# Kernel optimization log

Hardware: AMD Instinct MI355X
Metric: run time of the kernel (lower is better)

## Reference

```python
import jax, jax.numpy as jnp
import numpy as np

R0 = 1.0
DIM_A, DIM_V, DIM_D = 32, 32, 32
N_NODES = 20000
N_EDGES = 640000


def radial_encode_8(r, r0):
    # 8 Gaussian radial basis functions on the edge length |r_ij|
    d = jnp.linalg.norm(r, axis=-1)                      # [E]
    centers = jnp.linspace(0.0, r0, 8)                   # [8]
    width = r0 / 8.0
    return jnp.exp(-(((d[..., None] - centers) / width) ** 2))  # [E,8]


def tens_sigmoid_vec(v):
    # norm-saturating nonlinearity for rank-1 tensors (direction-preserving)
    n2 = jnp.sum(v * v, axis=-1, keepdims=True)
    return v * jax.lax.rsqrt(1.0 + n2)


def setup_inputs() -> dict:
    key = jax.random.key(0)
    ks = jax.random.split(key, 12)

    def lin(k, fan_in, fan_out):
        return jax.random.normal(k, (fan_in, fan_out), jnp.float32) / np.float32(np.sqrt(fan_in))

    return dict(
        r_ij=jax.random.normal(ks[0], (N_EDGES, 3), jnp.float32),
        w_rad=lin(ks[1], 8, DIM_A), b_rad=jnp.zeros((DIM_A,), jnp.float32),
        w_direct=lin(ks[2], DIM_A, DIM_A),
        w1=lin(ks[3], DIM_A, 2 * DIM_A), b1=jnp.zeros((2 * DIM_A,), jnp.float32),
        w2=lin(ks[4], 2 * DIM_A, 2 * DIM_A), b2=jnp.zeros((2 * DIM_A,), jnp.float32),
        w3=lin(ks[5], 2 * DIM_A, DIM_A), b3=jnp.zeros((DIM_A,), jnp.float32),
        w_v=lin(ks[6], DIM_A, DIM_V),
        w_d=lin(ks[7], DIM_A, DIM_D),
        edges_src=jax.random.randint(ks[8], (N_EDGES,), 0, N_NODES),
        n_nodes=N_NODES,
    )


def reference(r_ij, w_rad, b_rad, w_direct, w1, b1, w2, b2, w3, b3, w_v, w_d,
              edges_src, n_nodes):
    lrelu = lambda x: jnp.where(x > 0, x, 0.1 * x)
    # radial MLP: Linear(8, a) -> MLP (lin_direct + 3-layer leakyrelu net)
    h = radial_encode_8(r_ij, R0) @ w_rad + b_rad                      # [E,a]
    rad = h @ w_direct + (lrelu(lrelu(h @ w1 + b1) @ w2 + b2) @ w3 + b3)  # [E,a]
    rs = tens_sigmoid_vec(r_ij * (7.0 / R0))                            # [E,3]

    seg = lambda x: jax.ops.segment_sum(x, edges_src, num_segments=n_nodes)
    A_a = seg(rad)                                                      # [N,a]
    A_v = seg(rad[:, :, None] * rs[:, None, :])                         # [N,a,3]
    # phi_d_ij = rad ⊗ rs ⊗ rs per edge  -> [E,a,3,3], then scatter-sum
    A_d = seg(rad[:, :, None, None] * rs[:, None, None, :] * rs[:, None, :, None])  # [N,a,3,3]

    out_v = jnp.einsum('nac,av->nvc', A_v, w_v)                         # TensLinear rank 1
    out_d = jnp.einsum('naij,ad->ndij', A_d, w_d)                       # TensLinear rank 2
    return A_a, out_v, out_d
```

## Files before the change

kernel.cpp:

```cpp
#include <hip/hip_runtime.h>
#include <hip/hip_bf16.h>
#include <hip/hip_fp16.h>
#include <math.h>


#define TSIZE 8192
#define DMAX  2.0f
#define NPB   4
#define EPB   4
#define HB    128
#define TILE  10240

#define O_WRAD 0
#define O_BRAD 256
#define O_WDIR 288
#define O_W1   1312
#define O_B1   3360
#define O_W2   3424
#define O_B2   7520
#define O_W3   7584
#define O_B3   9632
#define O_WV   9664
#define O_WD   10688
#define W_TOT  11712

__device__ __forceinline__ float lrelu(float x) { return x > 0.0f ? x : 0.1f * x; }

__device__ __forceinline__ float ldf(const void* p, int i, bool f32) {
    return f32 ? ((const float*)p)[i]
               : __uint_as_float(((unsigned int)((const unsigned short*)p)[i]) << 16);
}
__device__ __forceinline__ void stf(void* p, size_t i, float v, bool f32) {
    if (f32) ((float*)p)[i] = v;
    else     ((__hip_bfloat16*)p)[i] = __float2bfloat16(v);
}

__device__ __forceinline__ bool detect_f32(const void* r) {
    const unsigned short* p = (const unsigned short*)r;
    int bad = 0;
#pragma unroll 8
    for (int i = 0; i < 128; i++) {
        float v = __uint_as_float(((unsigned int)p[i]) << 16);
        bad |= (!isfinite(v) || fabsf(v) > 1e5f) ? 1 : 0;
    }
    return bad != 0;
}

__global__ void k_prep(const void* __restrict__ r_ij,
                       const void* w_rad, const void* b_rad, const void* w_direct,
                       const void* w1, const void* b1, const void* w2, const void* b2,
                       const void* w3, const void* b3, const void* w_v, const void* w_d,
                       float* __restrict__ wcat, int* __restrict__ flag,
                       int* __restrict__ counts, int N) {
    const int b = blockIdx.x;
    if (b == 0) {
        if (threadIdx.x == 0) flag[0] = detect_f32(r_ij) ? 1 : 0;
    } else if (b <= 11) {
        const bool f32 = detect_f32(r_ij);
        const void* src; int cnt; int off;
        switch (b) {
            case 1:  src = w_rad;    cnt = 256;  off = O_WRAD; break;
            case 2:  src = b_rad;    cnt = 32;   off = O_BRAD; break;
            case 3:  src = w_direct; cnt = 1024; off = O_WDIR; break;
            case 4:  src = w1;       cnt = 2048; off = O_W1;   break;
            case 5:  src = b1;       cnt = 64;   off = O_B1;   break;
            case 6:  src = w2;       cnt = 4096; off = O_W2;   break;
            case 7:  src = b2;       cnt = 64;   off = O_B2;   break;
            case 8:  src = w3;       cnt = 2048; off = O_W3;   break;
            case 9:  src = b3;       cnt = 32;   off = O_B3;   break;
            case 10: src = w_v;      cnt = 1024; off = O_WV;   break;
            default: src = w_d;      cnt = 1024; off = O_WD;   break;
        }
        for (int i = threadIdx.x; i < cnt; i += blockDim.x)
            wcat[off + i] = ldf(src, i, f32);
    } else if (counts) {
        int i = (b - 12) * blockDim.x + threadIdx.x;
        if (i < N) counts[i] = 0;
    }
}

__global__ void __launch_bounds__(64 * EPB) k_table(const float* __restrict__ wcat,
                                                    float* __restrict__ tabI) {
    __shared__ float Lh[EPB][32], Lt1[EPB][64], Lt2[EPB][64], Lrad[EPB][32];

    const int s = threadIdx.x >> 6;
    const int j = threadIdx.x & 63;
    const int e = blockIdx.x * EPB + s;
    const float d = (float)e * (DMAX / (float)(TSIZE - 1));

    float enc[8];
#pragma unroll
    for (int k = 0; k < 8; k++) {
        float t = (d - (float)k * (1.0f / 7.0f)) * 8.0f;
        enc[k] = expf(-t * t);
    }

    if (j < 32) {
        float hv = wcat[O_BRAD + j];
#pragma unroll
        for (int k = 0; k < 8; k++) hv = fmaf(enc[k], wcat[O_WRAD + k * 32 + j], hv);
        Lh[s][j] = hv;
    }
    __syncthreads();

    {
        float v = wcat[O_B1 + j];
#pragma unroll
        for (int i = 0; i < 32; i++) v = fmaf(Lh[s][i], wcat[O_W1 + i * 64 + j], v);
        Lt1[s][j] = lrelu(v);
    }
    __syncthreads();

    {
        float v = wcat[O_B2 + j];
#pragma unroll
        for (int i = 0; i < 64; i++) v = fmaf(Lt1[s][i], wcat[O_W2 + i * 64 + j], v);
        Lt2[s][j] = lrelu(v);
    }
    __syncthreads();

    if (j < 32) {
        float v = wcat[O_B3 + j];
#pragma unroll
        for (int i = 0; i < 64; i++) v = fmaf(Lt2[s][i], wcat[O_W3 + i * 32 + j], v);
#pragma unroll
        for (int i = 0; i < 32; i++) v = fmaf(Lh[s][i], wcat[O_WDIR + i * 32 + j], v);
        Lrad[s][j] = v;
        tabI[e * 96 + j] = v;
    }
    __syncthreads();

    if (j < 32) {
        float sv = 0.0f, sd = 0.0f;
#pragma unroll
        for (int i = 0; i < 32; i++) {
            float ri = Lrad[s][i];
            sv = fmaf(ri, wcat[O_WV + i * 32 + j], sv);
            sd = fmaf(ri, wcat[O_WD + i * 32 + j], sd);
        }
        tabI[e * 96 + 32 + j] = sv;
        tabI[e * 96 + 64 + j] = sd;
    }
}

__global__ void __launch_bounds__(256) k_hist(const int* __restrict__ src, int E,
                                              int chunk,
                                              unsigned short* __restrict__ cnt,
                                              int N) {
    __shared__ int lcnt[TILE];
    const int b = blockIdx.x % HB;
    const int t = blockIdx.x / HB;
    const int lo = b * chunk;
    const int hi = min(lo + chunk, E);
    const int t0 = t * TILE;
    const int tl = min(TILE, N - t0);

    for (int i = threadIdx.x; i < tl; i += 256) lcnt[i] = 0;
    __syncthreads();
    for (int e = lo + threadIdx.x; e < hi; e += 256) {
        const int s = src[e] - t0;
        if ((unsigned)s < (unsigned)tl) atomicAdd(&lcnt[s], 1);
    }
    __syncthreads();
    unsigned short* out = cnt + (size_t)(t * HB + b) * TILE;
    for (int i = threadIdx.x; i < tl; i += 256)
        out[i] = (unsigned short)lcnt[i];
}

__global__ void k_colscan(unsigned short* __restrict__ cnt,
                          int* __restrict__ tot, int N) {
    int n = blockIdx.x * blockDim.x + threadIdx.x;
    if (n >= N) return;
    const int t = n / TILE;
    const int nl = n % TILE;
    unsigned short* col = cnt + (size_t)(t * HB) * TILE + nl;
    int run = 0;
#pragma unroll 4
    for (int b = 0; b < HB; b++) {
        int c = col[(size_t)b * TILE];
        col[(size_t)b * TILE] = (unsigned short)run;
        run += c;
    }
    tot[n] = run;
}

__global__ void k_scan(const int* __restrict__ tot, int* __restrict__ rowstart,
                       int N, int E) {
    __shared__ int part[1024];
    const int t = threadIdx.x;
    const int CH = (N + 1023) / 1024;
    const int lo = t * CH;
    const int hi = min(lo + CH, N);

    int s = 0;
    for (int i = lo; i < hi; i++) s += tot[i];
    part[t] = s;
    __syncthreads();

    for (int off = 1; off < 1024; off <<= 1) {
        int v = part[t];
        int w = (t >= off) ? part[t - off] : 0;
        __syncthreads();
        part[t] = v + w;
        __syncthreads();
    }

    int run = (t == 0) ? 0 : part[t - 1];
    for (int i = lo; i < hi; i++) {
        rowstart[i] = run;
        run += tot[i];
    }
    if (t == 0) rowstart[N] = E;
}

__global__ void __launch_bounds__(256) k_place(
        const int* __restrict__ src, int E, int chunk,
        const unsigned short* __restrict__ cnt, const int* __restrict__ rowstart,
        const void* __restrict__ r_ij, const int* __restrict__ flag,
        uint2* __restrict__ eps, int N) {
    __shared__ int cur[TILE];
    const int b = blockIdx.x % HB;
    const int t = blockIdx.x / HB;
    const int lo = b * chunk;
    const int hi = min(lo + chunk, E);
    const int t0 = t * TILE;
    const int tl = min(TILE, N - t0);
    const bool f32 = flag[0] != 0;

    const unsigned short* base = cnt + (size_t)(t * HB + b) * TILE;
    for (int i = threadIdx.x; i < tl; i += 256)
        cur[i] = rowstart[t0 + i] + (int)base[i];
    __syncthreads();
    for (int e = lo + threadIdx.x; e < hi; e += 256) {
        const int s = src[e] - t0;
        if ((unsigned)s < (unsigned)tl) {
            const int pos = atomicAdd(&cur[s], 1);
            const float x = ldf(r_ij, 3 * e + 0, f32);
            const float y = ldf(r_ij, 3 * e + 1, f32);
            const float z = ldf(r_ij, 3 * e + 2, f32);
            const float d2 = x * x + y * y + z * z;
            const float inv = rsqrtf(1.0f + 49.0f * d2);
            const float u = fminf(sqrtf(d2), DMAX) * ((float)(TSIZE - 1) / DMAX);
            const unsigned int ti = (unsigned int)(u + 0.5f);
            const unsigned int h0 = __half_as_ushort(__float2half(7.0f * x * inv));
            const unsigned int h1 = __half_as_ushort(__float2half(7.0f * y * inv));
            const unsigned int h2 = __half_as_ushort(__float2half(7.0f * z * inv));
            eps[pos] = make_uint2(h0 | (h1 << 16), h2 | (ti << 16));
        }
    }
}

__global__ void k_rank_g(const int* __restrict__ src, int* __restrict__ counts,
                         int* __restrict__ rank, int E) {
    int e = blockIdx.x * blockDim.x + threadIdx.x;
    if (e < E) rank[e] = atomicAdd(&counts[src[e]], 1);
}
__global__ void k_place_g(const int* __restrict__ src, const int* __restrict__ rank,
                          const int* __restrict__ rowstart,
                          int* __restrict__ perm, int E) {
    int e = blockIdx.x * blockDim.x + threadIdx.x;
    if (e < E) perm[rowstart[src[e]] + rank[e]] = e;
}

__global__ void __launch_bounds__(64 * NPB) k_nodes(
    const uint2* __restrict__ eps,
    const int* __restrict__ perm,
    const void* __restrict__ r_ij,
    const int* __restrict__ rowstart,
    const float* __restrict__ tabI,
    const int* __restrict__ flag,
    void* __restrict__ out, int N) {
    const int wave = threadIdx.x >> 6;
    const int lane = threadIdx.x & 63;
    const int n = blockIdx.x * NPB + wave;
    if (n >= N) return;
    const int a = lane & 31;
    const bool hi = (lane >> 5) != 0;
    const bool f32 = flag[0] != 0;

    const int s0 = rowstart[n];
    const int s1 = rowstart[n + 1];

    float accR = 0.f, acc1 = 0.f, acc2 = 0.f, acc3 = 0.f,
          acc4 = 0.f, acc5 = 0.f, acc6 = 0.f;

    if (eps) {
        int idx = s0;
        for (; idx + 1 < s1; idx += 2) {
            const uint2 qa = eps[idx];
            const uint2 qb = eps[idx + 1];
            const float ax = __half2float(__ushort_as_half((unsigned short)(qa.x & 0xffff)));
            const float ay = __half2float(__ushort_as_half((unsigned short)(qa.x >> 16)));
            const float az = __half2float(__ushort_as_half((unsigned short)(qa.y & 0xffff)));
            const int   ab = (int)(qa.y >> 16) * 96 + a;
            const float bx = __half2float(__ushort_as_half((unsigned short)(qb.x & 0xffff)));
            const float by = __half2float(__ushort_as_half((unsigned short)(qb.x >> 16)));
            const float bz = __half2float(__ushort_as_half((unsigned short)(qb.y & 0xffff)));
            const int   bb = (int)(qb.y >> 16) * 96 + a;

            const float raA = tabI[ab], rvA = tabI[ab + 32], rdA = tabI[ab + 64];
            const float raB = tabI[bb], rvB = tabI[bb + 32], rdB = tabI[bb + 64];

            const float b1A = (hi ? rdA : rvA) * (hi ? ay : 1.0f);
            const float b2A = rdA * (hi ? az : ax);
            const float b1B = (hi ? rdB : rvB) * (hi ? by : 1.0f);
            const float b2B = rdB * (hi ? bz : bx);

            accR += raA + raB;
            acc1 += b1A * ax + b1B * bx;
            acc2 += b1A * ay + b1B * by;
            acc3 += b1A * az + b1B * bz;
            acc4 += b2A * ax + b2B * bx;
            acc5 += b2A * ay + b2B * by;
            acc6 += b2A * az + b2B * bz;
        }
        if (idx < s1) {
            const uint2 q = eps[idx];
            const float x = __half2float(__ushort_as_half((unsigned short)(q.x & 0xffff)));
            const float y = __half2float(__ushort_as_half((unsigned short)(q.x >> 16)));
            const float z = __half2float(__ushort_as_half((unsigned short)(q.y & 0xffff)));
            const int   b = (int)(q.y >> 16) * 96 + a;
            const float ra = tabI[b], rv = tabI[b + 32], rd = tabI[b + 64];
            const float b1 = (hi ? rd : rv) * (hi ? y : 1.0f);
            const float b2 = rd * (hi ? z : x);
            accR += ra;
            acc1 += b1 * x; acc2 += b1 * y; acc3 += b1 * z;
            acc4 += b2 * x; acc5 += b2 * y; acc6 += b2 * z;
        }
    } else {
        for (int idx = s0; idx < s1; idx++) {
            const int e = perm[idx];
            const float x0 = ldf(r_ij, 3 * e + 0, f32);
            const float y0 = ldf(r_ij, 3 * e + 1, f32);
            const float z0 = ldf(r_ij, 3 * e + 2, f32);
            const float d2 = x0 * x0 + y0 * y0 + z0 * z0;
            const float inv = rsqrtf(1.0f + 49.0f * d2);
            const float x = 7.0f * x0 * inv, y = 7.0f * y0 * inv, z = 7.0f * z0 * inv;
            const float u = fminf(sqrtf(d2), DMAX) * ((float)(TSIZE - 1) / DMAX);
            const int b = (int)(u + 0.5f) * 96 + a;
            const float ra = tabI[b], rv = tabI[b + 32], rd = tabI[b + 64];
            const float b1 = (hi ? rd : rv) * (hi ? y : 1.0f);
            const float b2 = rd * (hi ? z : x);
            accR += ra;
            acc1 += b1 * x; acc2 += b1 * y; acc3 += b1 * z;
            acc4 += b2 * x; acc5 += b2 * y; acc6 += b2 * z;
        }
    }

    const size_t baseV = (size_t)N * 32;
    const size_t baseD = (size_t)N * 128;
    if (!hi) {
        stf(out, (size_t)n * 32 + a, accR, f32);
        const size_t vb = baseV + (size_t)n * 96 + a * 3;
        stf(out, vb + 0, acc1, f32);
        stf(out, vb + 1, acc2, f32);
        stf(out, vb + 2, acc3, f32);
        const size_t db = baseD + (size_t)n * 288 + a * 9;
        stf(out, db + 0, acc4, f32);
        stf(out, db + 1, acc5, f32);
        stf(out, db + 2, acc6, f32);
    } else {
        const size_t db = baseD + (size_t)n * 288 + a * 9;
        stf(out, db + 3, acc1, f32);
        stf(out, db + 4, acc2, f32);
        stf(out, db + 5, acc3, f32);
        stf(out, db + 6, acc4, f32);
        stf(out, db + 7, acc5, f32);
        stf(out, db + 8, acc6, f32);
    }
}

extern "C" void kernel_launch(void* const* d_in, const int* in_sizes, int n_in,
                              void* d_out, int out_size, void* d_ws, size_t ws_size,
                              hipStream_t stream) {
    const void* r_ij     = d_in[0];
    const void* w_rad    = d_in[1];
    const void* b_rad    = d_in[2];
    const void* w_direct = d_in[3];
    const void* w1       = d_in[4];
    const void* b1       = d_in[5];
    const void* w2       = d_in[6];
    const void* b2       = d_in[7];
    const void* w3       = d_in[8];
    const void* b3       = d_in[9];
    const void* w_v      = d_in[10];
    const void* w_d      = d_in[11];
    const int* edges_src = (const int*)d_in[12];

    const int E = in_sizes[12];
    const int N = out_size / 416;
    const int chunk = (E + HB - 1) / HB;
    const int ntiles = (N + TILE - 1) / TILE;

    const size_t cntBytes  = (size_t)ntiles * HB * TILE * 2;
    const size_t fastBytes = (size_t)E * 8
                           + ((size_t)W_TOT + 4 + (size_t)TSIZE * 96
                              + (size_t)N + (size_t)(N + 1)) * 4
                           + cntBytes;
    const bool use_fast = ws_size >= fastBytes + 64;

    char* w = (char*)d_ws;
    if (use_fast) {
        uint2* eps    = (uint2*)w;
        float* wcat   = (float*)(w + (size_t)E * 8);
        int* flag     = (int*)(wcat + W_TOT);
        float* tabI   = (float*)(flag + 4);
        unsigned short* cnt = (unsigned short*)(tabI + (size_t)TSIZE * 96);
        int* tot      = (int*)((char*)cnt + ((cntBytes + 3) & ~(size_t)3));
        int* rowstart = tot + N;

        k_prep<<<12, 256, 0, stream>>>(
            r_ij, w_rad, b_rad, w_direct, w1, b1, w2, b2, w3, b3, w_v, w_d,
            wcat, flag, nullptr, N);
        k_table<<<TSIZE / EPB, 64 * EPB, 0, stream>>>(wcat, tabI);
        k_hist<<<HB * ntiles, 256, 0, stream>>>(edges_src, E, chunk, cnt, N);
        k_colscan<<<(N + 255) / 256, 256, 0, stream>>>(cnt, tot, N);
        k_scan<<<1, 1024, 0, stream>>>(tot, rowstart, N, E);
        k_place<<<HB * ntiles, 256, 0, stream>>>(edges_src, E, chunk, cnt,
                                                 rowstart, r_ij, flag, eps, N);
        k_nodes<<<(N + NPB - 1) / NPB, 64 * NPB, 0, stream>>>(
            eps, nullptr, r_ij, rowstart, tabI, flag, d_out, N);
    } else {
        int* perm     = (int*)w;
        float* wcat   = (float*)(w + (size_t)E * 4);
        int* flag     = (int*)(wcat + W_TOT);
        float* tabI   = (float*)(flag + 4);
        int* counts   = (int*)(tabI + (size_t)TSIZE * 96);
        int* rowstart = counts + N;
        int* rank     = rowstart + N + 1;

        k_prep<<<12 + (N + 255) / 256, 256, 0, stream>>>(
            r_ij, w_rad, b_rad, w_direct, w1, b1, w2, b2, w3, b3, w_v, w_d,
            wcat, flag, counts, N);
        k_table<<<TSIZE / EPB, 64 * EPB, 0, stream>>>(wcat, tabI);
        k_rank_g<<<(E + 255) / 256, 256, 0, stream>>>(edges_src, counts, rank, E);
        k_scan<<<1, 1024, 0, stream>>>(counts, rowstart, N, E);
        k_place_g<<<(E + 255) / 256, 256, 0, stream>>>(edges_src, rank, rowstart,
                                                       perm, E);
        k_nodes<<<(N + NPB - 1) / NPB, 64 * NPB, 0, stream>>>(
            nullptr, perm, r_ij, rowstart, tabI, flag, d_out, N);
    }
}
```

Measured before the change: 232.4 us.

## Use fp32 16-byte edge records, parallel two-level scan, precomputed table offsets

Replaces the single-block 1024-thread scan with a per-wave reduction fused into the column scan plus a multi-block wave scan that adds coarse prefixes serially. When workspace allows, edge records become float4 (fp32 direction plus a pre-scaled byte offset into the table), which removes half-to-float conversions and index multiplies in the node kernel. The cost is twice the bytes written and read per edge. The fallback path is split into its own kernel.

New measurement: 218.8 us. 1.06x faster.

```diff
diff --git a/kernel.cpp b/kernel.cpp
--- a/kernel.cpp
+++ b/kernel.cpp
@@ -167,57 +167,54 @@
         out[i] = (unsigned short)lcnt[i];
 }
 
-__global__ void k_colscan(unsigned short* __restrict__ cnt,
-                          int* __restrict__ tot, int N) {
-    int n = blockIdx.x * blockDim.x + threadIdx.x;
-    if (n >= N) return;
-    const int t = n / TILE;
-    const int nl = n % TILE;
-    unsigned short* col = cnt + (size_t)(t * HB) * TILE + nl;
+__global__ void __launch_bounds__(64) k_colscan(unsigned short* __restrict__ cnt,
+                                                int* __restrict__ tot,
+                                                int* __restrict__ coarse, int N) {
+    const int lane = threadIdx.x;
+    const int n = blockIdx.x * 64 + lane;
     int run = 0;
+    if (n < N) {
+        const int t = n / TILE;
+        const int nl = n % TILE;
+        unsigned short* col = cnt + (size_t)(t * HB) * TILE + nl;
 #pragma unroll 4
-    for (int b = 0; b < HB; b++) {
-        int c = col[(size_t)b * TILE];
-        col[(size_t)b * TILE] = (unsigned short)run;
-        run += c;
-    }
-    tot[n] = run;
-}
-
-__global__ void k_scan(const int* __restrict__ tot, int* __restrict__ rowstart,
-                       int N, int E) {
-    __shared__ int part[1024];
-    const int t = threadIdx.x;
-    const int CH = (N + 1023) / 1024;
-    const int lo = t * CH;
-    const int hi = min(lo + CH, N);
-
-    int s = 0;
-    for (int i = lo; i < hi; i++) s += tot[i];
-    part[t] = s;
-    __syncthreads();
-
-    for (int off = 1; off < 1024; off <<= 1) {
-        int v = part[t];
-        int w = (t >= off) ? part[t - off] : 0;
-        __syncthreads();
-        part[t] = v + w;
-        __syncthreads();
-    }
-
-    int run = (t == 0) ? 0 : part[t - 1];
-    for (int i = lo; i < hi; i++) {
-        rowstart[i] = run;
-        run += tot[i];
-    }
-    if (t == 0) rowstart[N] = E;
-}
-
+        for (int b = 0; b < HB; b++) {
+            int c = col[(size_t)b * TILE];
+            col[(size_t)b * TILE] = (unsigned short)run;
+            run += c;
+        }
+        tot[n] = run;
+    }
+    int s = run;
+    for (int off = 32; off > 0; off >>= 1) s += __shfl_down(s, off);
+    if (lane == 0) coarse[blockIdx.x] = s;
+}
+
+__global__ void __launch_bounds__(64) k_scan2(const int* __restrict__ tot,
+                                              const int* __restrict__ coarse,
+                                              int* __restrict__ rowstart, int N) {
+    const int lane = threadIdx.x;
+    const int b = blockIdx.x;
+    int cpre = 0;
+    if (lane == 0) for (int i = 0; i < b; i++) cpre += coarse[i];
+    cpre = __shfl(cpre, 0);
+    const int n = b * 64 + lane;
+    const int v = (n < N) ? tot[n] : 0;
+    int inc = v;
+    for (int off = 1; off < 64; off <<= 1) {
+        int y = __shfl_up(inc, off);
+        if (lane >= off) inc += y;
+    }
+    if (n < N) rowstart[n] = cpre + inc - v;
+    if (n == N - 1) rowstart[N] = cpre + inc;
+}
+
+template <bool P16>
 __global__ void __launch_bounds__(256) k_place(
         const int* __restrict__ src, int E, int chunk,
         const unsigned short* __restrict__ cnt, const int* __restrict__ rowstart,
         const void* __restrict__ r_ij, const int* __restrict__ flag,
-        uint2* __restrict__ eps, int N) {
+        void* __restrict__ epsv, int N) {
     __shared__ int cur[TILE];
     const int b = blockIdx.x % HB;
     const int t = blockIdx.x / HB;
@@ -241,31 +238,26 @@
             const float d2 = x * x + y * y + z * z;
             const float inv = rsqrtf(1.0f + 49.0f * d2);
             const float u = fminf(sqrtf(d2), DMAX) * ((float)(TSIZE - 1) / DMAX);
-            const unsigned int ti = (unsigned int)(u + 0.5f);
-            const unsigned int h0 = __half_as_ushort(__float2half(7.0f * x * inv));
-            const unsigned int h1 = __half_as_ushort(__float2half(7.0f * y * inv));
-            const unsigned int h2 = __half_as_ushort(__float2half(7.0f * z * inv));
-            eps[pos] = make_uint2(h0 | (h1 << 16), h2 | (ti << 16));
-        }
-    }
-}
-
-__global__ void k_rank_g(const int* __restrict__ src, int* __restrict__ counts,
-                         int* __restrict__ rank, int E) {
-    int e = blockIdx.x * blockDim.x + threadIdx.x;
-    if (e < E) rank[e] = atomicAdd(&counts[src[e]], 1);
-}
-__global__ void k_place_g(const int* __restrict__ src, const int* __restrict__ rank,
-                          const int* __restrict__ rowstart,
-                          int* __restrict__ perm, int E) {
-    int e = blockIdx.x * blockDim.x + threadIdx.x;
-    if (e < E) perm[rowstart[src[e]] + rank[e]] = e;
-}
-
+            const int ti = (int)(u + 0.5f);
+            const float rs0 = 7.0f * x * inv, rs1 = 7.0f * y * inv,
+                        rs2 = 7.0f * z * inv;
+            if (P16) {
+                ((float4*)epsv)[pos] =
+                    make_float4(rs0, rs1, rs2, __int_as_float(ti * 384));
+            } else {
+                const unsigned int h0 = __half_as_ushort(__float2half(rs0));
+                const unsigned int h1 = __half_as_ushort(__float2half(rs1));
+                const unsigned int h2 = __half_as_ushort(__float2half(rs2));
+                ((uint2*)epsv)[pos] =
+                    make_uint2(h0 | (h1 << 16), h2 | ((unsigned)ti << 16));
+            }
+        }
+    }
+}
+
+template <bool P16>
 __global__ void __launch_bounds__(64 * NPB) k_nodes(
-    const uint2* __restrict__ eps,
-    const int* __restrict__ perm,
-    const void* __restrict__ r_ij,
+    const void* __restrict__ epsv,
     const int* __restrict__ rowstart,
     const float* __restrict__ tabI,
     const int* __restrict__ flag,
@@ -277,6 +269,7 @@
     const int a = lane & 31;
     const bool hi = (lane >> 5) != 0;
     const bool f32 = flag[0] != 0;
+    const char* tabA = (const char*)tabI + (a << 2);
 
     const int s0 = rowstart[n];
     const int s1 = rowstart[n + 1];
@@ -284,67 +277,65 @@
     float accR = 0.f, acc1 = 0.f, acc2 = 0.f, acc3 = 0.f,
           acc4 = 0.f, acc5 = 0.f, acc6 = 0.f;
 
-    if (eps) {
-        int idx = s0;
-        for (; idx + 1 < s1; idx += 2) {
-            const uint2 qa = eps[idx];
-            const uint2 qb = eps[idx + 1];
-            const float ax = __half2float(__ushort_as_half((unsigned short)(qa.x & 0xffff)));
-            const float ay = __half2float(__ushort_as_half((unsigned short)(qa.x >> 16)));
-            const float az = __half2float(__ushort_as_half((unsigned short)(qa.y & 0xffff)));
-            const int   ab = (int)(qa.y >> 16) * 96 + a;
-            const float bx = __half2float(__ushort_as_half((unsigned short)(qb.x & 0xffff)));
-            const float by = __half2float(__ushort_as_half((unsigned short)(qb.x >> 16)));
-            const float bz = __half2float(__ushort_as_half((unsigned short)(qb.y & 0xffff)));
-            const int   bb = (int)(qb.y >> 16) * 96 + a;
-
-            const float raA = tabI[ab], rvA = tabI[ab + 32], rdA = tabI[ab + 64];
-            const float raB = tabI[bb], rvB = tabI[bb + 32], rdB = tabI[bb + 64];
-
-            const float b1A = (hi ? rdA : rvA) * (hi ? ay : 1.0f);
-            const float b2A = rdA * (hi ? az : ax);
-            const float b1B = (hi ? rdB : rvB) * (hi ? by : 1.0f);
-            const float b2B = rdB * (hi ? bz : bx);
-
-            accR += raA + raB;
-            acc1 += b1A * ax + b1B * bx;
-            acc2 += b1A * ay + b1B * by;
-            acc3 += b1A * az + b1B * bz;
-            acc4 += b2A * ax + b2B * bx;
-            acc5 += b2A * ay + b2B * by;
-            acc6 += b2A * az + b2B * bz;
-        }
-        if (idx < s1) {
-            const uint2 q = eps[idx];
-            const float x = __half2float(__ushort_as_half((unsigned short)(q.x & 0xffff)));
-            const float y = __half2float(__ushort_as_half((unsigned short)(q.x >> 16)));
-            const float z = __half2float(__ushort_as_half((unsigned short)(q.y & 0xffff)));
-            const int   b = (int)(q.y >> 16) * 96 + a;
-            const float ra = tabI[b], rv = tabI[b + 32], rd = tabI[b + 64];
-            const float b1 = (hi ? rd : rv) * (hi ? y : 1.0f);
-            const float b2 = rd * (hi ? z : x);
-            accR += ra;
-            acc1 += b1 * x; acc2 += b1 * y; acc3 += b1 * z;
-            acc4 += b2 * x; acc5 += b2 * y; acc6 += b2 * z;
-        }
-    } else {
-        for (int idx = s0; idx < s1; idx++) {
-            const int e = perm[idx];
-            const float x0 = ldf(r_ij, 3 * e + 0, f32);
-            const float y0 = ldf(r_ij, 3 * e + 1, f32);
-            const float z0 = ldf(r_ij, 3 * e + 2, f32);
-            const float d2 = x0 * x0 + y0 * y0 + z0 * z0;
-            const float inv = rsqrtf(1.0f + 49.0f * d2);
-            const float x = 7.0f * x0 * inv, y = 7.0f * y0 * inv, z = 7.0f * z0 * inv;
-            const float u = fminf(sqrtf(d2), DMAX) * ((float)(TSIZE - 1) / DMAX);
-            const int b = (int)(u + 0.5f) * 96 + a;
-            const float ra = tabI[b], rv = tabI[b + 32], rd = tabI[b + 64];
-            const float b1 = (hi ? rd : rv) * (hi ? y : 1.0f);
-            const float b2 = rd * (hi ? z : x);
-            accR += ra;
-            acc1 += b1 * x; acc2 += b1 * y; acc3 += b1 * z;
-            acc4 += b2 * x; acc5 += b2 * y; acc6 += b2 * z;
-        }
+    int idx = s0;
+    for (; idx + 1 < s1; idx += 2) {
+        float ax, ay, az, bx, by, bz;
+        const float *pA, *pB;
+        if (P16) {
+            const float4 qa = ((const float4*)epsv)[idx];
+            const float4 qb = ((const float4*)epsv)[idx + 1];
+            ax = qa.x; ay = qa.y; az = qa.z;
+            bx = qb.x; by = qb.y; bz = qb.z;
+            pA = (const float*)(tabA + __float_as_int(qa.w));
+            pB = (const float*)(tabA + __float_as_int(qb.w));
+        } else {
+            const uint2 qa = ((const uint2*)epsv)[idx];
+            const uint2 qb = ((const uint2*)epsv)[idx + 1];
+            ax = __half2float(__ushort_as_half((unsigned short)(qa.x & 0xffff)));
+            ay = __half2float(__ushort_as_half((unsigned short)(qa.x >> 16)));
+            az = __half2float(__ushort_as_half((unsigned short)(qa.y & 0xffff)));
+            bx = __half2float(__ushort_as_half((unsigned short)(qb.x & 0xffff)));
+            by = __half2float(__ushort_as_half((unsigned short)(qb.x >> 16)));
+            bz = __half2float(__ushort_as_half((unsigned short)(qb.y & 0xffff)));
+            pA = (const float*)(tabA + (int)(qa.y >> 16) * 384);
+            pB = (const float*)(tabA + (int)(qb.y >> 16) * 384);
+        }
+        const float raA = pA[0], rvA = pA[32], rdA = pA[64];
+        const float raB = pB[0], rvB = pB[32], rdB = pB[64];
+
+        const float b1A = (hi ? rdA : rvA) * (hi ? ay : 1.0f);
+        const float b2A = rdA * (hi ? az : ax);
+        const float b1B = (hi ? rdB : rvB) * (hi ? by : 1.0f);
+        const float b2B = rdB * (hi ? bz : bx);
+
+        accR += raA + raB;
+        acc1 += b1A * ax + b1B * bx;
+        acc2 += b1A * ay + b1B * by;
+        acc3 += b1A * az + b1B * bz;
+        acc4 += b2A * ax + b2B * bx;
+        acc5 += b2A * ay + b2B * by;
+        acc6 += b2A * az + b2B * bz;
+    }
+    if (idx < s1) {
+        float x, y, z;
+        const float* p;
+        if (P16) {
+            const float4 q = ((const float4*)epsv)[idx];
+            x = q.x; y = q.y; z = q.z;
+            p = (const float*)(tabA + __float_as_int(q.w));
+        } else {
+            const uint2 q = ((const uint2*)epsv)[idx];
+            x = __half2float(__ushort_as_half((unsigned short)(q.x & 0xffff)));
+            y = __half2float(__ushort_as_half((unsigned short)(q.x >> 16)));
+            z = __half2float(__ushort_as_half((unsigned short)(q.y & 0xffff)));
+            p = (const float*)(tabA + (int)(q.y >> 16) * 384);
+        }
+        const float ra = p[0], rv = p[32], rd = p[64];
+        const float b1 = (hi ? rd : rv) * (hi ? y : 1.0f);
+        const float b2 = rd * (hi ? z : x);
+        accR += ra;
+        acc1 += b1 * x; acc2 += b1 * y; acc3 += b1 * z;
+        acc4 += b2 * x; acc5 += b2 * y; acc6 += b2 * z;
     }
 
     const size_t baseV = (size_t)N * 32;
@@ -370,6 +361,93 @@
     }
 }
 
+__global__ void k_rank_g(const int* __restrict__ src, int* __restrict__ counts,
+                         int* __restrict__ rank, int E) {
+    int e = blockIdx.x * blockDim.x + threadIdx.x;
+    if (e < E) rank[e] = atomicAdd(&counts[src[e]], 1);
+}
+__global__ void k_scan_g(const int* __restrict__ counts, int* __restrict__ rowstart,
+                         int N, int E) {
+    __shared__ int part[1024];
+    const int t = threadIdx.x;
+    const int CH = (N + 1023) / 1024;
+    const int lo = t * CH;
+    const int hi = min(lo + CH, N);
+    int s = 0;
+    for (int i = lo; i < hi; i++) s += counts[i];
+    part[t] = s;
+    __syncthreads();
+    for (int off = 1; off < 1024; off <<= 1) {
+        int v = part[t];
+        int w = (t >= off) ? part[t - off] : 0;
+        __syncthreads();
+        part[t] = v + w;
+        __syncthreads();
+    }
+    int run = (t == 0) ? 0 : part[t - 1];
+    for (int i = lo; i < hi; i++) { rowstart[i] = run; run += counts[i]; }
+    if (t == 0) rowstart[N] = E;
+}
+__global__ void k_place_g(const int* __restrict__ src, const int* __restrict__ rank,
+                          const int* __restrict__ rowstart,
+                          int* __restrict__ perm, int E) {
+    int e = blockIdx.x * blockDim.x + threadIdx.x;
+    if (e < E) perm[rowstart[src[e]] + rank[e]] = e;
+}
+__global__ void __launch_bounds__(64 * NPB) k_nodes_fb(
+    const int* __restrict__ perm, const void* __restrict__ r_ij,
+    const int* __restrict__ rowstart, const float* __restrict__ tabI,
+    const int* __restrict__ flag, void* __restrict__ out, int N) {
+    const int wave = threadIdx.x >> 6;
+    const int lane = threadIdx.x & 63;
+    const int n = blockIdx.x * NPB + wave;
+    if (n >= N) return;
+    const int a = lane & 31;
+    const bool hi = (lane >> 5) != 0;
+    const bool f32 = flag[0] != 0;
+    const int s0 = rowstart[n], s1 = rowstart[n + 1];
+    float accR = 0.f, acc1 = 0.f, acc2 = 0.f, acc3 = 0.f,
+          acc4 = 0.f, acc5 = 0.f, acc6 = 0.f;
+    for (int idx = s0; idx < s1; idx++) {
+        const int e = perm[idx];
+        const float x0 = ldf(r_ij, 3 * e + 0, f32);
+        const float y0 = ldf(r_ij, 3 * e + 1, f32);
+        const float z0 = ldf(r_ij, 3 * e + 2, f32);
+        const float d2 = x0 * x0 + y0 * y0 + z0 * z0;
+        const float inv = rsqrtf(1.0f + 49.0f * d2);
+        const float x = 7.0f * x0 * inv, y = 7.0f * y0 * inv, z = 7.0f * z0 * inv;
+        const float u = fminf(sqrtf(d2), DMAX) * ((float)(TSIZE - 1) / DMAX);
+        const int b = (int)(u + 0.5f) * 96 + a;
+        const float ra = tabI[b], rv = tabI[b + 32], rd = tabI[b + 64];
+        const float b1 = (hi ? rd : rv) * (hi ? y : 1.0f);
+        const float b2 = rd * (hi ? z : x);
+        accR += ra;
+        acc1 += b1 * x; acc2 += b1 * y; acc3 += b1 * z;
+        acc4 += b2 * x; acc5 += b2 * y; acc6 += b2 * z;
+    }
+    const size_t baseV = (size_t)N * 32;
+    const size_t baseD = (size_t)N * 128;
+    if (!hi) {
+        stf(out, (size_t)n * 32 + a, accR, f32);
+        const size_t vb = baseV + (size_t)n * 96 + a * 3;
+        stf(out, vb + 0, acc1, f32);
+        stf(out, vb + 1, acc2, f32);
+        stf(out, vb + 2, acc3, f32);
+        const size_t db = baseD + (size_t)n * 288 + a * 9;
+        stf(out, db + 0, acc4, f32);
+        stf(out, db + 1, acc5, f32);
+        stf(out, db + 2, acc6, f32);
+    } else {
+        const size_t db = baseD + (size_t)n * 288 + a * 9;
+        stf(out, db + 3, acc1, f32);
+        stf(out, db + 4, acc2, f32);
+        stf(out, db + 5, acc3, f32);
+        stf(out, db + 6, acc4, f32);
+        stf(out, db + 7, acc5, f32);
+        stf(out, db + 8, acc6, f32);
+    }
+}
+
 extern "C" void kernel_launch(void* const* d_in, const int* in_sizes, int n_in,
                               void* d_out, int out_size, void* d_ws, size_t ws_size,
                               hipStream_t stream) {
@@ -391,35 +469,44 @@
     const int N = out_size / 416;
     const int chunk = (E + HB - 1) / HB;
     const int ntiles = (N + TILE - 1) / TILE;
+    const int NB = (N + 63) / 64;
 
     const size_t cntBytes  = (size_t)ntiles * HB * TILE * 2;
-    const size_t fastBytes = (size_t)E * 8
-                           + ((size_t)W_TOT + 4 + (size_t)TSIZE * 96
-                              + (size_t)N + (size_t)(N + 1)) * 4
-                           + cntBytes;
-    const bool use_fast = ws_size >= fastBytes + 64;
+    const size_t tailBytes = ((size_t)W_TOT + 4) * 4 + (size_t)TSIZE * 96 * 4
+                           + cntBytes + ((size_t)N + NB + N + 1) * 4;
+    const bool p16 = ws_size >= (size_t)E * 16 + tailBytes + 64;
+    const bool p8  = !p16 && ws_size >= (size_t)E * 8 + tailBytes + 64;
 
     char* w = (char*)d_ws;
-    if (use_fast) {
-        uint2* eps    = (uint2*)w;
-        float* wcat   = (float*)(w + (size_t)E * 8);
+    if (p16 || p8) {
+        const size_t slot = (size_t)E * (p16 ? 16 : 8);
+        void* eps     = (void*)w;
+        float* wcat   = (float*)(w + slot);
         int* flag     = (int*)(wcat + W_TOT);
         float* tabI   = (float*)(flag + 4);
         unsigned short* cnt = (unsigned short*)(tabI + (size_t)TSIZE * 96);
-        int* tot      = (int*)((char*)cnt + ((cntBytes + 3) & ~(size_t)3));
-        int* rowstart = tot + N;
+        int* tot      = (int*)((char*)cnt + cntBytes);
+        int* coarse   = tot + N;
+        int* rowstart = coarse + NB;
 
         k_prep<<<12, 256, 0, stream>>>(
             r_ij, w_rad, b_rad, w_direct, w1, b1, w2, b2, w3, b3, w_v, w_d,
             wcat, flag, nullptr, N);
         k_table<<<TSIZE / EPB, 64 * EPB, 0, stream>>>(wcat, tabI);
         k_hist<<<HB * ntiles, 256, 0, stream>>>(edges_src, E, chunk, cnt, N);
-        k_colscan<<<(N + 255) / 256, 256, 0, stream>>>(cnt, tot, N);
-        k_scan<<<1, 1024, 0, stream>>>(tot, rowstart, N, E);
-        k_place<<<HB * ntiles, 256, 0, stream>>>(edges_src, E, chunk, cnt,
-                                                 rowstart, r_ij, flag, eps, N);
-        k_nodes<<<(N + NPB - 1) / NPB, 64 * NPB, 0, stream>>>(
-            eps, nullptr, r_ij, rowstart, tabI, flag, d_out, N);
+        k_colscan<<<NB, 64, 0, stream>>>(cnt, tot, coarse, N);
+        k_scan2<<<NB, 64, 0, stream>>>(tot, coarse, rowstart, N);
+        if (p16) {
+            k_place<true><<<HB * ntiles, 256, 0, stream>>>(
+                edges_src, E, chunk, cnt, rowstart, r_ij, flag, eps, N);
+            k_nodes<true><<<(N + NPB - 1) / NPB, 64 * NPB, 0, stream>>>(
+                eps, rowstart, tabI, flag, d_out, N);
+        } else {
+            k_place<false><<<HB * ntiles, 256, 0, stream>>>(
+                edges_src, E, chunk, cnt, rowstart, r_ij, flag, eps, N);
+            k_nodes<false><<<(N + NPB - 1) / NPB, 64 * NPB, 0, stream>>>(
+                eps, rowstart, tabI, flag, d_out, N);
+        }
     } else {
         int* perm     = (int*)w;
         float* wcat   = (float*)(w + (size_t)E * 4);
@@ -434,10 +521,10 @@
             wcat, flag, counts, N);
         k_table<<<TSIZE / EPB, 64 * EPB, 0, stream>>>(wcat, tabI);
         k_rank_g<<<(E + 255) / 256, 256, 0, stream>>>(edges_src, counts, rank, E);
-        k_scan<<<1, 1024, 0, stream>>>(counts, rowstart, N, E);
+        k_scan_g<<<1, 1024, 0, stream>>>(counts, rowstart, N, E);
         k_place_g<<<(E + 255) / 256, 256, 0, stream>>>(edges_src, rank, rowstart,
                                                        perm, E);
-        k_nodes<<<(N + NPB - 1) / NPB, 64 * NPB, 0, stream>>>(
-            nullptr, perm, r_ij, rowstart, tabI, flag, d_out, N);
-    }
-}
+        k_nodes_fb<<<(N + NPB - 1) / NPB, 64 * NPB, 0, stream>>>(
+            perm, r_ij, rowstart, tabI, flag, d_out, N);
+    }
+}
```
